# Performance work log

Hardware: AMD Instinct MI355X
Metric: run time of the kernel (lower is better)

The kernel has to match this reference:

```python
import jax, jax.numpy as jnp
import numpy as np

B, D, N, K = 8, 3, 65536, 64
EPS = 1e-8

def setup_inputs() -> dict:
    key = jax.random.key(0)
    k1, k2, k3 = jax.random.split(key, 3)
    return {
        "template_features": jax.random.normal(k1, (B, D, N), dtype=jnp.float32),
        "source_features": jax.random.normal(k2, (B, D, N), dtype=jnp.float32),
        "W": jax.random.normal(k3, (D, K), dtype=jnp.float32),
    }

def _gamma(features_t, W):
    # features_t: (B,N,D); logits: (B,K,N); softmax over points (dim=2, as in torch code)
    logits = jnp.einsum('bnd,dk->bkn', features_t, W)
    return jax.nn.softmax(logits, axis=2)

def _gmm_params(gamma, pts):
    # gamma: (B,K,N), pts: (B,N,D)
    n = gamma.shape[2]
    Npi = gamma.sum(axis=2) + EPS                       # (B,K)
    pi = Npi / n
    g = gamma / (Npi[:, :, None] + EPS)                 # (B,K,N)
    mu = jnp.einsum('bkn,bnd->bkd', g, pts)             # weighted mean
    # second moment; exact central form: sum_n g (x-mu)(x-mu)^T = Exx - (2 - s) mu mu^T
    Exx = jnp.einsum('bkn,bnd,bne->bkde', g, pts, pts)
    s = g.sum(axis=2)                                   # (B,K), ~1 (not exactly, due to eps)
    outer = mu[..., :, None] * mu[..., None, :]
    sigma = (Exx - (2.0 - s)[..., None, None] * outer) / (Npi[:, :, None, None] + EPS)
    return pi, mu, sigma

def _estimate_transform(mu_x, pi_x, mu_y, pi_y):
    cx = jnp.sum(mu_x * pi_x[..., None], axis=1, keepdims=True)   # (B,1,D)
    cy = jnp.sum(mu_y * pi_y[..., None], axis=1, keepdims=True)
    mu_x_c = mu_x - cx
    mu_y_c = mu_y - cy
    Wm = jnp.einsum('bkd,bke->bde', pi_x[..., None] * mu_y_c, mu_x_c)  # (B,D,D)
    U, S, Vh = jnp.linalg.svd(Wm, full_matrices=False)
    R = jnp.matmul(U, Vh)
    det = jnp.linalg.det(R)
    Vh = Vh.at[:, :, -1].multiply(jnp.sign(det)[:, None])
    R = jnp.matmul(U, Vh)
    T = cy[:, 0, :] - jnp.einsum('bde,be->bd', R, cx[:, 0, :])
    return R, T

def reference(template_features, source_features, W):
    template_pts = jnp.swapaxes(template_features, 1, 2)   # (B,N,D)
    source_pts = jnp.swapaxes(source_features, 1, 2)
    t_gamma = _gamma(template_pts, W)
    s_gamma = _gamma(source_pts, W)
    t_pi, t_mu, t_sigma = _gmm_params(t_gamma, template_pts)
    s_pi, s_mu, s_sigma = _gmm_params(s_gamma, source_pts)
    R, T = _estimate_transform(s_mu, s_pi, t_mu, t_pi)
    aligned = jnp.matmul(source_pts, jnp.swapaxes(R, 1, 2)) + T[:, None, :]
    return aligned
```

## Files before the change

kernel.cpp:

```cpp
#include <hip/hip_runtime.h>

#define N_PTS 65536
#define BATCH 8
#define KCL   64
#define LOG2E 1.44269504088896340736f

__device__ __forceinline__ double drcp(double x) {
    double r = (double)(1.0f / (float)x);
    r = r * (2.0 - x * r);
    r = r * (2.0 - x * r);
    return r;
}

__device__ __forceinline__ float hw_exp2(float x) {
    return __builtin_amdgcn_exp2f(x);
}

__global__ __launch_bounds__(256) void k_sum(const float* __restrict__ tmpl,
                                             const float* __restrict__ srcf,
                                             const float* __restrict__ Wmat,
                                             float* __restrict__ Zs,
                                             float* __restrict__ Ss) {
    const int tid  = threadIdx.x;
    const int lane = tid & 63;
    const int wv   = tid >> 6;

    const int gw  = __builtin_amdgcn_readfirstlane(blockIdx.x * 4 + wv);
    const int set = gw >> 10;
    const int b   = (gw >> 7) & 7;
    const int n0  = (gw & 127) * 512;
    const float* bp = (set ? srcf : tmpl) + (size_t)b * 3 * N_PTS + n0;

    const float w0 = Wmat[lane] * LOG2E;
    const float w1 = Wmat[KCL + lane] * LOG2E;
    const float w2 = Wmat[2 * KCL + lane] * LOG2E;

    float z = 0.f, s0 = 0.f, s1 = 0.f, s2 = 0.f;
    const float4* p0 = (const float4*)bp;
    const float4* p1 = (const float4*)(bp + N_PTS);
    const float4* p2 = (const float4*)(bp + 2 * N_PTS);
#pragma unroll 4
    for (int q = 0; q < 128; ++q) {
        float4 a = p0[q];
        float4 c = p1[q];
        float4 d = p2[q];
        {
            float l = fmaf(a.x, w0, fmaf(c.x, w1, d.x * w2));
            float e = hw_exp2(l);
            z += e; s0 = fmaf(e, a.x, s0); s1 = fmaf(e, c.x, s1); s2 = fmaf(e, d.x, s2);
        }
        {
            float l = fmaf(a.y, w0, fmaf(c.y, w1, d.y * w2));
            float e = hw_exp2(l);
            z += e; s0 = fmaf(e, a.y, s0); s1 = fmaf(e, c.y, s1); s2 = fmaf(e, d.y, s2);
        }
        {
            float l = fmaf(a.z, w0, fmaf(c.z, w1, d.z * w2));
            float e = hw_exp2(l);
            z += e; s0 = fmaf(e, a.z, s0); s1 = fmaf(e, c.z, s1); s2 = fmaf(e, d.z, s2);
        }
        {
            float l = fmaf(a.w, w0, fmaf(c.w, w1, d.w * w2));
            float e = hw_exp2(l);
            z += e; s0 = fmaf(e, a.w, s0); s1 = fmaf(e, c.w, s1); s2 = fmaf(e, d.w, s2);
        }
    }

    __shared__ float red[4][KCL][4];
    red[wv][lane][0] = z;
    red[wv][lane][1] = s0;
    red[wv][lane][2] = s1;
    red[wv][lane][3] = s2;
    __syncthreads();
    if (tid < KCL) {
        float rz  = red[0][tid][0] + red[1][tid][0] + red[2][tid][0] + red[3][tid][0];
        float rs0 = red[0][tid][1] + red[1][tid][1] + red[2][tid][1] + red[3][tid][1];
        float rs1 = red[0][tid][2] + red[1][tid][2] + red[2][tid][2] + red[3][tid][2];
        float rs2 = red[0][tid][3] + red[1][tid][3] + red[2][tid][3] + red[3][tid][3];
        int idx = (set * BATCH + b) * KCL + tid;
        atomicAdd(&Zs[idx], rz);
        atomicAdd(&Ss[idx * 3 + 0], rs0);
        atomicAdd(&Ss[idx * 3 + 1], rs1);
        atomicAdd(&Ss[idx * 3 + 2], rs2);
    }
}

__global__ __launch_bounds__(256) void k_apply(const float* __restrict__ srcf,
                                               const float* __restrict__ Zs,
                                               const float* __restrict__ Ss,
                                               float* __restrict__ out) {
    __shared__ float rt_s[BATCH][12];

    if (threadIdx.x < 64) {
        const int lane = threadIdx.x;
        const int b    = lane >> 3;
        const int sub  = lane & 7;

        const double inv_npi = 1.0 / (1.0 + 2e-8);
        const double pi_c = (1.0 + 1e-8) / (double)N_PTS;

        double Mt[3] = {0, 0, 0}, Ms[3] = {0, 0, 0};
        double P[3][3] = {{0,0,0},{0,0,0},{0,0,0}};
        for (int kk = 0; kk < 8; ++kk) {
            int k  = sub * 8 + kk;
            int it = b * KCL + k;
            int is = (BATCH + b) * KCL + k;
            double izt = inv_npi * drcp((double)Zs[it]);
            double izs = inv_npi * drcp((double)Zs[is]);
            double mt[3], ms[3];
            for (int d = 0; d < 3; ++d) {
                mt[d] = (double)Ss[it * 3 + d] * izt;
                ms[d] = (double)Ss[is * 3 + d] * izs;
                Mt[d] += mt[d];
                Ms[d] += ms[d];
            }
            for (int d = 0; d < 3; ++d)
                for (int e = 0; e < 3; ++e)
                    P[d][e] += mt[d] * ms[e];
        }
        for (int m = 1; m <= 4; m <<= 1) {
            for (int d = 0; d < 3; ++d) {
                Mt[d] += __shfl_xor(Mt[d], m, 64);
                Ms[d] += __shfl_xor(Ms[d], m, 64);
            }
            for (int d = 0; d < 3; ++d)
                for (int e = 0; e < 3; ++e)
                    P[d][e] += __shfl_xor(P[d][e], m, 64);
        }

        double cy[3], cx[3];
        for (int d = 0; d < 3; ++d) { cy[d] = pi_c * Mt[d]; cx[d] = pi_c * Ms[d]; }

        const double coef = 2.0 * pi_c - 64.0 * pi_c * pi_c;
        double A[3][3];
        for (int d = 0; d < 3; ++d)
            for (int e = 0; e < 3; ++e)
                A[d][e] = pi_c * (P[d][e] - coef * Mt[d] * Ms[e]);

        double G[3][3];
        for (int i = 0; i < 3; ++i)
            for (int j = 0; j < 3; ++j) {
                double acc = 0;
                for (int d = 0; d < 3; ++d) acc += A[d][i] * A[d][j];
                G[i][j] = acc;
            }

        double V[3][3] = {{1,0,0},{0,1,0},{0,0,1}};
        const int pairs[3][2] = {{0,1},{0,2},{1,2}};
        const double scale0 = fabs(G[0][0]) + fabs(G[1][1]) + fabs(G[2][2]) + 1e-300;
        for (int sweep = 0; sweep < 10; ++sweep) {
            double off = fabs(G[0][1]) + fabs(G[0][2]) + fabs(G[1][2]);
            if (off < 1e-28 * scale0) break;
            for (int pi_i = 0; pi_i < 3; ++pi_i) {
                int p = pairs[pi_i][0], q = pairs[pi_i][1];
                double apq = G[p][q];
                if (fabs(apq) < 1e-30 * scale0) continue;
                double tau = (G[q][q] - G[p][p]) * drcp(2.0 * apq);
                double t = ((tau >= 0) ? 1.0 : -1.0) * drcp(fabs(tau) + sqrt(1.0 + tau * tau));
                double c = drcp(sqrt(1.0 + t * t));
                double s = t * c;
                double gpp = G[p][p], gqq = G[q][q];
                G[p][p] = gpp - t * apq;
                G[q][q] = gqq + t * apq;
                G[p][q] = G[q][p] = 0.0;
                int r = 3 - p - q;
                double grp = G[r][p], grq = G[r][q];
                G[r][p] = G[p][r] = c * grp - s * grq;
                G[r][q] = G[q][r] = s * grp + c * grq;
                for (int rr = 0; rr < 3; ++rr) {
                    double vrp = V[rr][p], vrq = V[rr][q];
                    V[rr][p] = c * vrp - s * vrq;
                    V[rr][q] = s * vrp + c * vrq;
                }
            }
        }

        double invs[3];
        for (int i = 0; i < 3; ++i) {
            double lam = G[i][i];
            invs[i] = drcp(sqrt(lam > 1e-300 ? lam : 1e-300));
        }
        double M[3][3];
        for (int i = 0; i < 3; ++i)
            for (int j = 0; j < 3; ++j) {
                double acc = 0;
                for (int m2 = 0; m2 < 3; ++m2) acc += V[i][m2] * V[j][m2] * invs[m2];
                M[i][j] = acc;
            }
        double R0[3][3];
        for (int d = 0; d < 3; ++d)
            for (int e = 0; e < 3; ++e) {
                double acc = 0;
                for (int m2 = 0; m2 < 3; ++m2) acc += A[d][m2] * M[m2][e];
                R0[d][e] = acc;
            }

        double det = R0[0][0] * (R0[1][1] * R0[2][2] - R0[1][2] * R0[2][1])
                   - R0[0][1] * (R0[1][0] * R0[2][2] - R0[1][2] * R0[2][0])
                   + R0[0][2] * (R0[1][0] * R0[2][1] - R0[1][1] * R0[2][0]);
        double sg = (det >= 0.0) ? 1.0 : -1.0;
        R0[0][2] *= sg; R0[1][2] *= sg; R0[2][2] *= sg;

        double T[3];
        for (int d = 0; d < 3; ++d)
            T[d] = cy[d] - (R0[d][0] * cx[0] + R0[d][1] * cx[1] + R0[d][2] * cx[2]);

        if (sub == 0) {
            rt_s[b][0] = (float)R0[0][0]; rt_s[b][1] = (float)R0[0][1]; rt_s[b][2] = (float)R0[0][2];
            rt_s[b][3] = (float)R0[1][0]; rt_s[b][4] = (float)R0[1][1]; rt_s[b][5] = (float)R0[1][2];
            rt_s[b][6] = (float)R0[2][0]; rt_s[b][7] = (float)R0[2][1]; rt_s[b][8] = (float)R0[2][2];
            rt_s[b][9] = (float)T[0]; rt_s[b][10] = (float)T[1]; rt_s[b][11] = (float)T[2];
        }
    }
    __syncthreads();

    const int t = blockIdx.x * 256 + threadIdx.x;
#pragma unroll
    for (int i = 0; i < 4; ++i) {
        int idx = t + i * 131072;
        int b = idx >> 16;
        int n = idx & (N_PTS - 1);
        const float* rt = rt_s[b];
        const float* base = srcf + (size_t)b * 3 * N_PTS;
        float x0 = base[n];
        float x1 = base[N_PTS + n];
        float x2 = base[2 * N_PTS + n];
        float y0 = fmaf(rt[0], x0, fmaf(rt[1], x1, fmaf(rt[2], x2, rt[9])));
        float y1 = fmaf(rt[3], x0, fmaf(rt[4], x1, fmaf(rt[5], x2, rt[10])));
        float y2 = fmaf(rt[6], x0, fmaf(rt[7], x1, fmaf(rt[8], x2, rt[11])));
        size_t o = (size_t)idx * 3;
        out[o + 0] = y0;
        out[o + 1] = y1;
        out[o + 2] = y2;
    }
}

extern "C" void kernel_launch(void* const* d_in, const int* in_sizes, int n_in,
                              void* d_out, int out_size, void* d_ws, size_t ws_size,
                              hipStream_t stream) {
    const float* tmpl = (const float*)d_in[0];
    const float* srcf = (const float*)d_in[1];
    const float* Wmat = (const float*)d_in[2];
    float* out = (float*)d_out;

    float* Zs = (float*)d_ws;
    float* Ss = (float*)d_ws + 1024;

    (void)hipMemsetAsync(d_ws, 0, 4096 * sizeof(float), stream);

    k_sum<<<512, 256, 0, stream>>>(tmpl, srcf, Wmat, Zs, Ss);
    k_apply<<<512, 256, 0, stream>>>(srcf, Zs, Ss, out);
}
```

Measured before the change: 100.7 us.

## Stage point chunks in LDS and use packed f32x2 math in k_sum

k_sum now stages each 1024-point chunk of the three coordinates into shared memory cooperatively, so the loads are coalesced. Each wave then reads its own slice from LDS as a broadcast, instead of every lane issuing the same global loads. The accumulation uses 2-wide vector FMAs so the compiler can emit packed FP32 instructions. The grid doubles to 1024 blocks to match the smaller per-block work. In exchange it adds a barrier and an LDS round trip, and the per-lane partial sums change slightly in order.

```diff
diff --git a/kernel.cpp b/kernel.cpp
--- a/kernel.cpp
+++ b/kernel.cpp
@@ -3,7 +3,11 @@
 #define N_PTS 65536
 #define BATCH 8
 #define KCL   64
+#define CHUNK 1024
 #define LOG2E 1.44269504088896340736f
+
+typedef float f32x2 __attribute__((ext_vector_type(2)));
+typedef float f32x4 __attribute__((ext_vector_type(4)));
 
 __device__ __forceinline__ double drcp(double x) {
     double r = (double)(1.0f / (float)x);
@@ -21,56 +25,66 @@
                                              const float* __restrict__ Wmat,
                                              float* __restrict__ Zs,
                                              float* __restrict__ Ss) {
-    const int tid  = threadIdx.x;
+    const int bx    = blockIdx.x;
+    const int set   = bx >> 9;
+    const int b     = (bx >> 6) & 7;
+    const int chunk = bx & 63;
+    const float* feat = set ? srcf : tmpl;
+    const int n0 = chunk * CHUNK;
+
+    __shared__ float xs[3][CHUNK];
+    __shared__ float red[4][KCL][4];
+
+    const int tid = threadIdx.x;
+    const float* base = feat + (size_t)b * 3 * N_PTS + n0;
+    for (int i = tid; i < 3 * (CHUNK / 4); i += 256) {
+        int d = i / (CHUNK / 4);
+        int p = i % (CHUNK / 4);
+        float4 v = ((const float4*)(base + (size_t)d * N_PTS))[p];
+        ((float4*)&xs[d][0])[p] = v;
+    }
+    __syncthreads();
+
     const int lane = tid & 63;
     const int wv   = tid >> 6;
-
-    const int gw  = __builtin_amdgcn_readfirstlane(blockIdx.x * 4 + wv);
-    const int set = gw >> 10;
-    const int b   = (gw >> 7) & 7;
-    const int n0  = (gw & 127) * 512;
-    const float* bp = (set ? srcf : tmpl) + (size_t)b * 3 * N_PTS + n0;
-
     const float w0 = Wmat[lane] * LOG2E;
     const float w1 = Wmat[KCL + lane] * LOG2E;
     const float w2 = Wmat[2 * KCL + lane] * LOG2E;
-
-    float z = 0.f, s0 = 0.f, s1 = 0.f, s2 = 0.f;
-    const float4* p0 = (const float4*)bp;
-    const float4* p1 = (const float4*)(bp + N_PTS);
-    const float4* p2 = (const float4*)(bp + 2 * N_PTS);
-#pragma unroll 4
-    for (int q = 0; q < 128; ++q) {
-        float4 a = p0[q];
-        float4 c = p1[q];
-        float4 d = p2[q];
+    const f32x2 w0v = {w0, w0}, w1v = {w1, w1}, w2v = {w2, w2};
+
+    f32x2 z2 = {0.f, 0.f}, s02 = {0.f, 0.f}, s12 = {0.f, 0.f}, s22 = {0.f, 0.f};
+    const int q0 = wv * (CHUNK / 16);
+#pragma unroll 2
+    for (int q = q0; q < q0 + CHUNK / 16; ++q) {
+        f32x4 a = ((const f32x4*)&xs[0][0])[q];
+        f32x4 c = ((const f32x4*)&xs[1][0])[q];
+        f32x4 d = ((const f32x4*)&xs[2][0])[q];
         {
-            float l = fmaf(a.x, w0, fmaf(c.x, w1, d.x * w2));
-            float e = hw_exp2(l);
-            z += e; s0 = fmaf(e, a.x, s0); s1 = fmaf(e, c.x, s1); s2 = fmaf(e, d.x, s2);
+            f32x2 ax = a.xy, cx = c.xy, dx = d.xy;
+            f32x2 l = __builtin_elementwise_fma(ax, w0v,
+                        __builtin_elementwise_fma(cx, w1v, dx * w2v));
+            f32x2 e = {hw_exp2(l.x), hw_exp2(l.y)};
+            z2 += e;
+            s02 = __builtin_elementwise_fma(e, ax, s02);
+            s12 = __builtin_elementwise_fma(e, cx, s12);
+            s22 = __builtin_elementwise_fma(e, dx, s22);
         }
         {
-            float l = fmaf(a.y, w0, fmaf(c.y, w1, d.y * w2));
-            float e = hw_exp2(l);
-            z += e; s0 = fmaf(e, a.y, s0); s1 = fmaf(e, c.y, s1); s2 = fmaf(e, d.y, s2);
-        }
-        {
-            float l = fmaf(a.z, w0, fmaf(c.z, w1, d.z * w2));
-            float e = hw_exp2(l);
-            z += e; s0 = fmaf(e, a.z, s0); s1 = fmaf(e, c.z, s1); s2 = fmaf(e, d.z, s2);
-        }
-        {
-            float l = fmaf(a.w, w0, fmaf(c.w, w1, d.w * w2));
-            float e = hw_exp2(l);
-            z += e; s0 = fmaf(e, a.w, s0); s1 = fmaf(e, c.w, s1); s2 = fmaf(e, d.w, s2);
-        }
-    }
-
-    __shared__ float red[4][KCL][4];
-    red[wv][lane][0] = z;
-    red[wv][lane][1] = s0;
-    red[wv][lane][2] = s1;
-    red[wv][lane][3] = s2;
+            f32x2 ax = a.zw, cx = c.zw, dx = d.zw;
+            f32x2 l = __builtin_elementwise_fma(ax, w0v,
+                        __builtin_elementwise_fma(cx, w1v, dx * w2v));
+            f32x2 e = {hw_exp2(l.x), hw_exp2(l.y)};
+            z2 += e;
+            s02 = __builtin_elementwise_fma(e, ax, s02);
+            s12 = __builtin_elementwise_fma(e, cx, s12);
+            s22 = __builtin_elementwise_fma(e, dx, s22);
+        }
+    }
+
+    red[wv][lane][0] = z2.x + z2.y;
+    red[wv][lane][1] = s02.x + s02.y;
+    red[wv][lane][2] = s12.x + s12.y;
+    red[wv][lane][3] = s22.x + s22.y;
     __syncthreads();
     if (tid < KCL) {
         float rz  = red[0][tid][0] + red[1][tid][0] + red[2][tid][0] + red[3][tid][0];
@@ -248,6 +262,6 @@
 
     (void)hipMemsetAsync(d_ws, 0, 4096 * sizeof(float), stream);
 
-    k_sum<<<512, 256, 0, stream>>>(tmpl, srcf, Wmat, Zs, Ss);
+    k_sum<<<1024, 256, 0, stream>>>(tmpl, srcf, Wmat, Zs, Ss);
     k_apply<<<512, 256, 0, stream>>>(srcf, Zs, Ss, out);
 }
```

Measured after the change: 92.95 us. 7.7% less time.
